# Performance work log

Hardware: AMD Instinct MI355X
Metric: run time of the kernel (lower is better)

## Reference

```python
import jax, jax.numpy as jnp
import numpy as np

B, S, H, NH = 4, 2048, 1024, 16
D = H // NH

def setup_inputs() -> dict:
    key = jax.random.key(0)
    ks = jax.random.split(key, 9)
    sc = 1.0 / np.sqrt(H)
    return {
        "x": jax.random.normal(ks[0], (B, S, H), jnp.float32),
        "Wq": jax.random.normal(ks[1], (H, H), jnp.float32) * sc,
        "bq": jax.random.normal(ks[2], (H,), jnp.float32) * 0.01,
        "Wk": jax.random.normal(ks[3], (H, H), jnp.float32) * sc,
        "bk": jax.random.normal(ks[4], (H,), jnp.float32) * 0.01,
        "Wv": jax.random.normal(ks[5], (H, H), jnp.float32) * sc,
        "bv": jax.random.normal(ks[6], (H,), jnp.float32) * 0.01,
        "Wo": jax.random.normal(ks[7], (H, H), jnp.float32) * sc,
        "bo": jax.random.normal(ks[8], (H,), jnp.float32) * 0.01,
    }

def reference(x, Wq, bq, Wk, bk, Wv, bv, Wo, bo):
    # torch Linear: y = x @ W.T + b
    def proj(x, W, b):
        # [B,S,H] -> [B,NH,S,D]
        y = jnp.einsum('bsh,oh->bso', x, W) + b
        return y.reshape(B, S, NH, D).transpose(0, 2, 1, 3)
    q = proj(x, Wq, bq)
    k = proj(x, Wk, bk)
    v = proj(x, Wv, bv)
    scores = jnp.einsum('bhqd,bhkd->bhqk', q, k) / jnp.sqrt(jnp.float32(D))
    p = jax.nn.softmax(scores, axis=-1)  # [B,NH,S,S]
    o = jnp.einsum('bhqk,bhkd->bhqd', p, v)  # dropout p=0 (eval)
    o = o.transpose(0, 2, 1, 3).reshape(B, S, H)
    return jnp.einsum('bsh,oh->bso', o, Wo) + bo
```

## Files before the change

kernel.cpp:

```cpp
#include <hip/hip_runtime.h>


#define DEV __device__ __forceinline__

typedef __bf16 bf16x8 __attribute__((ext_vector_type(8)));
typedef __bf16 bf16x4 __attribute__((ext_vector_type(4)));
typedef float floatx4 __attribute__((ext_vector_type(4)));

constexpr int Bdim = 4, SS = 2048, HH = 1024, NHH = 16, DD = 64;
constexpr int MM = Bdim * SS;

DEV void async16(const void* g, void* l) {
  __builtin_amdgcn_global_load_lds(
      (const __attribute__((address_space(1))) unsigned int*)g,
      (__attribute__((address_space(3))) unsigned int*)l, 16, 0, 0);
}

DEV int swz2(int r) { return (r ^ (r >> 2)) & 3; }
DEV int swz3(int r) { return (r ^ (r >> 3)) & 7; }

__global__ __launch_bounds__(256) void cast_bf16_kernel(
    const float* __restrict__ x, const float* __restrict__ wq,
    const float* __restrict__ wk, const float* __restrict__ wv,
    const float* __restrict__ wo,
    __bf16* __restrict__ xb, __bf16* __restrict__ wqb, __bf16* __restrict__ wkb,
    __bf16* __restrict__ wvb, __bf16* __restrict__ wob) {
  const float* src; __bf16* dst; int n4;
  switch (blockIdx.z) {
    case 0: src = x;  dst = xb;  n4 = MM * HH / 4; break;
    case 1: src = wq; dst = wqb; n4 = HH * HH / 4; break;
    case 2: src = wk; dst = wkb; n4 = HH * HH / 4; break;
    case 3: src = wv; dst = wvb; n4 = HH * HH / 4; break;
    default: src = wo; dst = wob; n4 = HH * HH / 4; break;
  }
  int stride = gridDim.x * blockDim.x;
  for (int i = blockIdx.x * blockDim.x + threadIdx.x; i < n4; i += stride) {
    float4 v = ((const float4*)src)[i];
    bf16x4 o;
    o[0] = (__bf16)v.x; o[1] = (__bf16)v.y; o[2] = (__bf16)v.z; o[3] = (__bf16)v.w;
    ((bf16x4*)dst)[i] = o;
  }
}

DEV void gemm128(const __bf16* __restrict__ Ablk, const __bf16* __restrict__ Bblk,
                 __bf16* As, __bf16* Bs, floatx4 acc[4][4]) {
  const int t = threadIdx.x;
  const int lane = t & 63, quad = lane >> 4, l16 = lane & 15;
  const int wid = t >> 6;
  const int wm = (wid >> 1) * 64, wn = (wid & 1) * 64;

  const int srow = t >> 2;
  const int sc = t & 3;
  const __bf16* Ag0 = Ablk + (size_t)srow * HH + (sc ^ swz2(srow)) * 8;
  const __bf16* Ag1 = Ablk + (size_t)(srow + 64) * HH + (sc ^ swz2(srow + 64)) * 8;
  const __bf16* Bg0 = Bblk + (size_t)srow * HH + (sc ^ swz2(srow)) * 8;
  const __bf16* Bg1 = Bblk + (size_t)(srow + 64) * HH + (sc ^ swz2(srow + 64)) * 8;
  __bf16* AsW = As + t * 8;
  __bf16* BsW = Bs + t * 8;

  int aoff[4], boff[4];
#pragma unroll
  for (int i = 0; i < 4; ++i) {
    int ra = wm + i * 16 + l16;
    aoff[i] = ra * 32 + (quad ^ swz2(ra)) * 8;
    int rb = wn + i * 16 + l16;
    boff[i] = rb * 32 + (quad ^ swz2(rb)) * 8;
  }

  for (int k0 = 0; k0 < HH; k0 += 32) {
    async16(Ag0 + k0, AsW);
    async16(Ag1 + k0, AsW + 2048);
    async16(Bg0 + k0, BsW);
    async16(Bg1 + k0, BsW + 2048);
    __syncthreads();
    bf16x8 af[4], bfr[4];
#pragma unroll
    for (int i = 0; i < 4; ++i) {
      af[i]  = *(const bf16x8*)&As[aoff[i]];
      bfr[i] = *(const bf16x8*)&Bs[boff[i]];
    }
#pragma unroll
    for (int mi = 0; mi < 4; ++mi)
#pragma unroll
      for (int ni = 0; ni < 4; ++ni)
        acc[mi][ni] = __builtin_amdgcn_mfma_f32_16x16x32_bf16(af[mi], bfr[ni],
                                                              acc[mi][ni], 0, 0, 0);
    __syncthreads();
  }
}

__global__ __launch_bounds__(256) void proj_qkv_kernel(
    const __bf16* __restrict__ xb,
    const __bf16* __restrict__ wqb, const __bf16* __restrict__ wkb,
    const __bf16* __restrict__ wvb,
    const float* __restrict__ bq, const float* __restrict__ bk,
    const float* __restrict__ bv,
    __bf16* __restrict__ Q, __bf16* __restrict__ Kc, __bf16* __restrict__ Vt) {
  __shared__ __align__(16) __bf16 As[128 * 32];
  __shared__ __align__(16) __bf16 Bs[128 * 32];
  const int mode = blockIdx.z;
  const __bf16* W = mode == 0 ? wqb : mode == 1 ? wkb : wvb;
  const float* bias = mode == 0 ? bq : mode == 1 ? bk : bv;
  const int m0 = blockIdx.y * 128, n0 = blockIdx.x * 128;

  floatx4 acc[4][4] = {};
  gemm128(xb + (size_t)m0 * HH, W + (size_t)n0 * HH, As, Bs, acc);

  const int t = threadIdx.x, lane = t & 63, quad = lane >> 4, l16 = lane & 15;
  const int wid = t >> 6, wm = (wid >> 1) * 64, wn = (wid & 1) * 64;
  const float qscale = 0.125f * 1.44269504088896f;
#pragma unroll
  for (int ni = 0; ni < 4; ++ni) {
    int n = n0 + wn + ni * 16 + l16;
    float bval = bias[n];
    int h = n >> 6, d = n & 63;
#pragma unroll
    for (int mi = 0; mi < 4; ++mi) {
#pragma unroll
      for (int r = 0; r < 4; ++r) {
        int m = m0 + wm + mi * 16 + quad * 4 + r;
        int bb = m >> 11, s = m & (SS - 1);
        float v = acc[mi][ni][r] + bval;
        size_t bh = (size_t)(bb * NHH + h);
        if (mode == 0)      Q [(bh * SS + s) * DD + d] = (__bf16)(v * qscale);
        else if (mode == 1) Kc[(bh * SS + s) * DD + d] = (__bf16)v;
        else                Vt[(bh * DD + d) * SS + s] = (__bf16)v;
      }
    }
  }
}

__global__ __launch_bounds__(256) void proj_out_kernel(
    const __bf16* __restrict__ Ob, const __bf16* __restrict__ wob,
    const float* __restrict__ bo, float* __restrict__ out) {
  __shared__ __align__(16) __bf16 As[128 * 32];
  __shared__ __align__(16) __bf16 Bs[128 * 32];
  const int m0 = blockIdx.y * 128, n0 = blockIdx.x * 128;
  floatx4 acc[4][4] = {};
  gemm128(Ob + (size_t)m0 * HH, wob + (size_t)n0 * HH, As, Bs, acc);
  const int t = threadIdx.x, lane = t & 63, quad = lane >> 4, l16 = lane & 15;
  const int wid = t >> 6, wm = (wid >> 1) * 64, wn = (wid & 1) * 64;
#pragma unroll
  for (int ni = 0; ni < 4; ++ni) {
    int n = n0 + wn + ni * 16 + l16;
    float bval = bo[n];
#pragma unroll
    for (int mi = 0; mi < 4; ++mi)
#pragma unroll
      for (int r = 0; r < 4; ++r) {
        int m = m0 + wm + mi * 16 + quad * 4 + r;
        out[(size_t)m * HH + n] = acc[mi][ni][r] + bval;
      }
  }
}

__global__ __launch_bounds__(256, 3) void attn_kernel(
    const __bf16* __restrict__ Q, const __bf16* __restrict__ Kc,
    const __bf16* __restrict__ Vt, __bf16* __restrict__ Ob) {
  __shared__ __align__(16) __bf16 Ks[2][64 * 64];
  __shared__ __align__(16) __bf16 Vs[2][64 * 64];
  __shared__ __align__(16) __bf16 Ps[4 * 32 * 72];

  const int t = threadIdx.x, lane = t & 63, quad = lane >> 4, l16 = lane & 15;
  const int wid = t >> 6;
  const int qt = blockIdx.x, h = blockIdx.y, b = blockIdx.z;
  const size_t bh = (size_t)b * NHH + h;
  const __bf16* Qg = Q + (bh * SS + (size_t)qt * 128) * DD;
  const __bf16* Kg = Kc + bh * SS * DD;
  const __bf16* Vg = Vt + bh * DD * SS;

  const int srow = t >> 3;
  const int sc = t & 7;

  const __bf16* KgA = Kg + (size_t)srow * DD + (sc ^ swz3(srow)) * 8;
  const __bf16* KgB = Kg + (size_t)(srow + 32) * DD + (sc ^ swz3(srow + 32)) * 8;
  const __bf16* VgA = Vg + (size_t)srow * SS + (sc ^ swz3(srow)) * 8;
  const __bf16* VgB = Vg + (size_t)(srow + 32) * SS + (sc ^ swz3(srow + 32)) * 8;

  bf16x8 qf[2][2];
#pragma unroll
  for (int ni = 0; ni < 2; ++ni)
#pragma unroll
    for (int ks = 0; ks < 2; ++ks)
      qf[ni][ks] = *(const bf16x8*)(Qg + (size_t)(wid * 32 + ni * 16 + l16) * DD
                                    + (ks * 4 + quad) * 8);

  floatx4 oacc[2][4] = {};
  float rsum[2] = {0.f, 0.f};

  __bf16* Pw = Ps + wid * (32 * 72);

  int koff[4][2];
#pragma unroll
  for (int mi = 0; mi < 4; ++mi) {
    int r = mi * 16 + l16;
#pragma unroll
    for (int ks = 0; ks < 2; ++ks)
      koff[mi][ks] = r * 64 + ((ks * 4 + quad) ^ swz3(r)) * 8;
  }

  async16(KgA, &Ks[0][t * 8]);
  async16(KgB, &Ks[0][2048 + t * 8]);
  async16(VgA, &Vs[0][t * 8]);
  async16(VgB, &Vs[0][2048 + t * 8]);

  for (int kt = 0; kt < SS / 64; ++kt) {
    const int cur = kt & 1;
    __syncthreads();

    if (kt + 1 < SS / 64) {
      const int kk = (kt + 1) * 64;
      const int nxt = cur ^ 1;
      async16(KgA + (size_t)kk * DD, &Ks[nxt][t * 8]);
      async16(KgB + (size_t)kk * DD, &Ks[nxt][2048 + t * 8]);
      async16(VgA + kk, &Vs[nxt][t * 8]);
      async16(VgB + kk, &Vs[nxt][2048 + t * 8]);
    }

    floatx4 sacc[4][2] = {};
#pragma unroll
    for (int ks = 0; ks < 2; ++ks) {
      bf16x8 kf[4];
#pragma unroll
      for (int mi = 0; mi < 4; ++mi) kf[mi] = *(const bf16x8*)&Ks[cur][koff[mi][ks]];
#pragma unroll
      for (int mi = 0; mi < 4; ++mi)
#pragma unroll
        for (int ni = 0; ni < 2; ++ni)
          sacc[mi][ni] = __builtin_amdgcn_mfma_f32_16x16x32_bf16(kf[mi], qf[ni][ks],
                                                                 sacc[mi][ni], 0, 0, 0);
    }

#pragma unroll
    for (int mi = 0; mi < 4; ++mi)
#pragma unroll
      for (int ni = 0; ni < 2; ++ni) {
        bf16x4 pk;
#pragma unroll
        for (int r = 0; r < 4; ++r) {
          float p = __builtin_amdgcn_exp2f(sacc[mi][ni][r]);
          rsum[ni] += p;
          pk[r] = (__bf16)p;
        }
        *(bf16x4*)&Pw[(ni * 16 + l16) * 72 + mi * 16 + quad * 4] = pk;
      }

#pragma unroll
    for (int ks = 0; ks < 2; ++ks) {
      bf16x8 ap[2], bv8[4];
#pragma unroll
      for (int mi = 0; mi < 2; ++mi)
        ap[mi] = *(const bf16x8*)&Pw[(mi * 16 + l16) * 72 + ks * 32 + quad * 8];
#pragma unroll
      for (int nj = 0; nj < 4; ++nj) bv8[nj] = *(const bf16x8*)&Vs[cur][koff[nj][ks]];
#pragma unroll
      for (int mi = 0; mi < 2; ++mi)
#pragma unroll
        for (int nj = 0; nj < 4; ++nj)
          oacc[mi][nj] = __builtin_amdgcn_mfma_f32_16x16x32_bf16(ap[mi], bv8[nj],
                                                                 oacc[mi][nj], 0, 0, 0);
    }
  }

#pragma unroll
  for (int ni = 0; ni < 2; ++ni) {
    rsum[ni] += __shfl_xor(rsum[ni], 16, 64);
    rsum[ni] += __shfl_xor(rsum[ni], 32, 64);
  }

  const int s0 = qt * 128 + wid * 32;
#pragma unroll
  for (int mi = 0; mi < 2; ++mi) {
#pragma unroll
    for (int r = 0; r < 4; ++r) {
      float inv = 1.f / __shfl(rsum[mi], quad * 4 + r, 64);
      int s = s0 + mi * 16 + quad * 4 + r;
#pragma unroll
      for (int nj = 0; nj < 4; ++nj) {
        int d = nj * 16 + l16;
        Ob[((size_t)b * SS + s) * HH + h * DD + d] = (__bf16)(oacc[mi][nj][r] * inv);
      }
    }
  }
}

extern "C" void kernel_launch(void* const* d_in, const int* in_sizes, int n_in,
                              void* d_out, int out_size, void* d_ws, size_t ws_size,
                              hipStream_t stream) {
  const float* x  = (const float*)d_in[0];
  const float* Wq = (const float*)d_in[1];
  const float* bq = (const float*)d_in[2];
  const float* Wk = (const float*)d_in[3];
  const float* bk = (const float*)d_in[4];
  const float* Wv = (const float*)d_in[5];
  const float* bv = (const float*)d_in[6];
  const float* Wo = (const float*)d_in[7];
  const float* bo = (const float*)d_in[8];
  float* out = (float*)d_out;

  char* ws = (char*)d_ws;
  __bf16* xb  = (__bf16*)(ws);
  __bf16* wqb = (__bf16*)(ws + 16777216);
  __bf16* wkb = (__bf16*)(ws + 18874368);
  __bf16* wvb = (__bf16*)(ws + 20971520);
  __bf16* wob = (__bf16*)(ws + 23068672);
  __bf16* Qb  = (__bf16*)(ws + 25165824);
  __bf16* Kb  = (__bf16*)(ws + 41943040);
  __bf16* Vtb = (__bf16*)(ws + 58720256);
  __bf16* Ob  = (__bf16*)(ws + 75497472);

  cast_bf16_kernel<<<dim3(256, 1, 5), 256, 0, stream>>>(x, Wq, Wk, Wv, Wo,
                                                        xb, wqb, wkb, wvb, wob);
  proj_qkv_kernel<<<dim3(8, 64, 3), 256, 0, stream>>>(xb, wqb, wkb, wvb,
                                                      bq, bk, bv, Qb, Kb, Vtb);
  attn_kernel<<<dim3(16, 16, 4), 256, 0, stream>>>(Qb, Kb, Vtb, Ob);
  proj_out_kernel<<<dim3(8, 64), 256, 0, stream>>>(Ob, wob, bo, out);
}
```

Measured before the change: 323.2 us.

## Double-buffer projection GEMM tiles and fuse QKV into one wide stacked-weight GEMM

Replaces the single-buffered 128x128 GEMM loop with a templated double-buffered version. It prefetches the next K-slice into a second LDS buffer while computing on the current one, which drops one barrier per iteration. The QKV projection now runs as one GEMM over the contiguous stacked Wq/Wk/Wv weights, using 128x256 tiles, and picks the head, mode and bias per output column. This is meant to hide global-load latency and improve A-tile reuse, at the cost of twice the LDS use, more accumulator registers and fewer blocks.

```diff
diff --git a/kernel.cpp b/kernel.cpp
--- a/kernel.cpp
+++ b/kernel.cpp
@@ -42,78 +42,94 @@
   }
 }
 
-DEV void gemm128(const __bf16* __restrict__ Ablk, const __bf16* __restrict__ Bblk,
-                 __bf16* As, __bf16* Bs, floatx4 acc[4][4]) {
+template <int TN>
+DEV void gemm_db(const __bf16* __restrict__ Ablk, const __bf16* __restrict__ Bblk,
+                 __bf16* As, __bf16* Bs, floatx4 acc[4][TN / 32]) {
+  constexpr int NF = TN / 32;
+  constexpr int BGRP = TN / 64;
+  constexpr int BBUF = TN * 32;
   const int t = threadIdx.x;
   const int lane = t & 63, quad = lane >> 4, l16 = lane & 15;
   const int wid = t >> 6;
-  const int wm = (wid >> 1) * 64, wn = (wid & 1) * 64;
-
-  const int srow = t >> 2;
-  const int sc = t & 3;
-  const __bf16* Ag0 = Ablk + (size_t)srow * HH + (sc ^ swz2(srow)) * 8;
-  const __bf16* Ag1 = Ablk + (size_t)(srow + 64) * HH + (sc ^ swz2(srow + 64)) * 8;
-  const __bf16* Bg0 = Bblk + (size_t)srow * HH + (sc ^ swz2(srow)) * 8;
-  const __bf16* Bg1 = Bblk + (size_t)(srow + 64) * HH + (sc ^ swz2(srow + 64)) * 8;
-  __bf16* AsW = As + t * 8;
-  __bf16* BsW = Bs + t * 8;
-
-  int aoff[4], boff[4];
+  const int wm = (wid >> 1) * 64, wn = (wid & 1) * (TN / 2);
+
+  const int srow = t >> 2, sc = t & 3;
+  const __bf16* Ag[2];
+  const __bf16* Bg[BGRP];
+#pragma unroll
+  for (int g = 0; g < 2; ++g)
+    Ag[g] = Ablk + (size_t)(srow + 64 * g) * HH + (sc ^ swz2(srow + 64 * g)) * 8;
+#pragma unroll
+  for (int g = 0; g < BGRP; ++g)
+    Bg[g] = Bblk + (size_t)(srow + 64 * g) * HH + (sc ^ swz2(srow + 64 * g)) * 8;
+
+  int aoff[4], boff[NF];
 #pragma unroll
   for (int i = 0; i < 4; ++i) {
     int ra = wm + i * 16 + l16;
     aoff[i] = ra * 32 + (quad ^ swz2(ra)) * 8;
+  }
+#pragma unroll
+  for (int i = 0; i < NF; ++i) {
     int rb = wn + i * 16 + l16;
     boff[i] = rb * 32 + (quad ^ swz2(rb)) * 8;
   }
 
-  for (int k0 = 0; k0 < HH; k0 += 32) {
-    async16(Ag0 + k0, AsW);
-    async16(Ag1 + k0, AsW + 2048);
-    async16(Bg0 + k0, BsW);
-    async16(Bg1 + k0, BsW + 2048);
+#pragma unroll
+  for (int g = 0; g < 2; ++g) async16(Ag[g], As + g * 2048 + t * 8);
+#pragma unroll
+  for (int g = 0; g < BGRP; ++g) async16(Bg[g], Bs + g * 2048 + t * 8);
+
+  for (int it = 0; it < HH / 32; ++it) {
+    const int cur = it & 1;
     __syncthreads();
-    bf16x8 af[4], bfr[4];
-#pragma unroll
-    for (int i = 0; i < 4; ++i) {
-      af[i]  = *(const bf16x8*)&As[aoff[i]];
-      bfr[i] = *(const bf16x8*)&Bs[boff[i]];
-    }
+
+    if (it + 1 < HH / 32) {
+      const int k = (it + 1) * 32;
+      const int nxt = cur ^ 1;
+#pragma unroll
+      for (int g = 0; g < 2; ++g)
+        async16(Ag[g] + k, As + nxt * 4096 + g * 2048 + t * 8);
+#pragma unroll
+      for (int g = 0; g < BGRP; ++g)
+        async16(Bg[g] + k, Bs + nxt * BBUF + g * 2048 + t * 8);
+    }
+
+    bf16x8 af[4], bfr[NF];
+#pragma unroll
+    for (int i = 0; i < 4; ++i) af[i] = *(const bf16x8*)&As[cur * 4096 + aoff[i]];
+#pragma unroll
+    for (int i = 0; i < NF; ++i) bfr[i] = *(const bf16x8*)&Bs[cur * BBUF + boff[i]];
 #pragma unroll
     for (int mi = 0; mi < 4; ++mi)
 #pragma unroll
-      for (int ni = 0; ni < 4; ++ni)
+      for (int ni = 0; ni < NF; ++ni)
         acc[mi][ni] = __builtin_amdgcn_mfma_f32_16x16x32_bf16(af[mi], bfr[ni],
                                                               acc[mi][ni], 0, 0, 0);
-    __syncthreads();
   }
 }
 
 __global__ __launch_bounds__(256) void proj_qkv_kernel(
-    const __bf16* __restrict__ xb,
-    const __bf16* __restrict__ wqb, const __bf16* __restrict__ wkb,
-    const __bf16* __restrict__ wvb,
+    const __bf16* __restrict__ xb, const __bf16* __restrict__ wstk,
     const float* __restrict__ bq, const float* __restrict__ bk,
     const float* __restrict__ bv,
     __bf16* __restrict__ Q, __bf16* __restrict__ Kc, __bf16* __restrict__ Vt) {
-  __shared__ __align__(16) __bf16 As[128 * 32];
-  __shared__ __align__(16) __bf16 Bs[128 * 32];
-  const int mode = blockIdx.z;
-  const __bf16* W = mode == 0 ? wqb : mode == 1 ? wkb : wvb;
-  const float* bias = mode == 0 ? bq : mode == 1 ? bk : bv;
-  const int m0 = blockIdx.y * 128, n0 = blockIdx.x * 128;
-
-  floatx4 acc[4][4] = {};
-  gemm128(xb + (size_t)m0 * HH, W + (size_t)n0 * HH, As, Bs, acc);
+  __shared__ __align__(16) __bf16 As[2 * 128 * 32];
+  __shared__ __align__(16) __bf16 Bs[2 * 256 * 32];
+  const int m0 = blockIdx.y * 128, n0 = blockIdx.x * 256;
+
+  floatx4 acc[4][8] = {};
+  gemm_db<256>(xb + (size_t)m0 * HH, wstk + (size_t)n0 * HH, As, Bs, acc);
 
   const int t = threadIdx.x, lane = t & 63, quad = lane >> 4, l16 = lane & 15;
-  const int wid = t >> 6, wm = (wid >> 1) * 64, wn = (wid & 1) * 64;
+  const int wid = t >> 6, wm = (wid >> 1) * 64, wn = (wid & 1) * 128;
   const float qscale = 0.125f * 1.44269504088896f;
 #pragma unroll
-  for (int ni = 0; ni < 4; ++ni) {
+  for (int ni = 0; ni < 8; ++ni) {
     int n = n0 + wn + ni * 16 + l16;
-    float bval = bias[n];
-    int h = n >> 6, d = n & 63;
+    int mode = n >> 10, nn = n & 1023;
+    int h = nn >> 6, d = nn & 63;
+    float bval = (mode == 0 ? bq : mode == 1 ? bk : bv)[nn];
 #pragma unroll
     for (int mi = 0; mi < 4; ++mi) {
 #pragma unroll
@@ -133,11 +149,11 @@
 __global__ __launch_bounds__(256) void proj_out_kernel(
     const __bf16* __restrict__ Ob, const __bf16* __restrict__ wob,
     const float* __restrict__ bo, float* __restrict__ out) {
-  __shared__ __align__(16) __bf16 As[128 * 32];
-  __shared__ __align__(16) __bf16 Bs[128 * 32];
+  __shared__ __align__(16) __bf16 As[2 * 128 * 32];
+  __shared__ __align__(16) __bf16 Bs[2 * 128 * 32];
   const int m0 = blockIdx.y * 128, n0 = blockIdx.x * 128;
   floatx4 acc[4][4] = {};
-  gemm128(Ob + (size_t)m0 * HH, wob + (size_t)n0 * HH, As, Bs, acc);
+  gemm_db<128>(Ob + (size_t)m0 * HH, wob + (size_t)n0 * HH, As, Bs, acc);
   const int t = threadIdx.x, lane = t & 63, quad = lane >> 4, l16 = lane & 15;
   const int wid = t >> 6, wm = (wid >> 1) * 64, wn = (wid & 1) * 64;
 #pragma unroll
@@ -311,8 +327,8 @@
 
   cast_bf16_kernel<<<dim3(256, 1, 5), 256, 0, stream>>>(x, Wq, Wk, Wv, Wo,
                                                         xb, wqb, wkb, wvb, wob);
-  proj_qkv_kernel<<<dim3(8, 64, 3), 256, 0, stream>>>(xb, wqb, wkb, wvb,
-                                                      bq, bk, bv, Qb, Kb, Vtb);
+  proj_qkv_kernel<<<dim3(12, 64), 256, 0, stream>>>(xb, wqb, bq, bk, bv,
+                                                    Qb, Kb, Vtb);
   attn_kernel<<<dim3(16, 16, 4), 256, 0, stream>>>(Qb, Kb, Vtb, Ob);
   proj_out_kernel<<<dim3(8, 64), 256, 0, stream>>>(Ob, wob, bo, out);
 }
```

Measured after the change: 355.4 us. +9.9%, slower.

## Double-buffer QKV GEMM, vectorize V stores, and enlarge attention query tile

Applied to the files above, without the earlier changes.

Adds a double-buffered LDS variant of the 128x128 GEMM for the QKV projection, issuing the next K-slice's async loads before computing on the current one, which removes one barrier per iteration. The transposed V epilogue now writes four contiguous bf16 values per store instead of scattered scalars. The attention kernel now gives each wave 64 query rows instead of 32, so each block covers 256 rows and K/V tiles loaded into LDS are reused across twice as many queries. This halves the grid. The cost is more registers, with occupancy lowered from 3 to 2 blocks, and P is processed in two 32-column halves through a smaller staging buffer.

```diff
diff --git a/kernel.cpp b/kernel.cpp
--- a/kernel.cpp
+++ b/kernel.cpp
@@ -42,6 +42,61 @@
   }
 }
 
+DEV void gemm_db128(const __bf16* __restrict__ Ablk, const __bf16* __restrict__ Bblk,
+                    __bf16* As, __bf16* Bs, floatx4 acc[4][4]) {
+  const int t = threadIdx.x;
+  const int lane = t & 63, quad = lane >> 4, l16 = lane & 15;
+  const int wid = t >> 6;
+  const int wm = (wid >> 1) * 64, wn = (wid & 1) * 64;
+
+  const int srow = t >> 2, sc = t & 3;
+  const __bf16* Ag0 = Ablk + (size_t)srow * HH + (sc ^ swz2(srow)) * 8;
+  const __bf16* Ag1 = Ablk + (size_t)(srow + 64) * HH + (sc ^ swz2(srow + 64)) * 8;
+  const __bf16* Bg0 = Bblk + (size_t)srow * HH + (sc ^ swz2(srow)) * 8;
+  const __bf16* Bg1 = Bblk + (size_t)(srow + 64) * HH + (sc ^ swz2(srow + 64)) * 8;
+
+  int aoff[4], boff[4];
+#pragma unroll
+  for (int i = 0; i < 4; ++i) {
+    int ra = wm + i * 16 + l16;
+    aoff[i] = ra * 32 + (quad ^ swz2(ra)) * 8;
+    int rb = wn + i * 16 + l16;
+    boff[i] = rb * 32 + (quad ^ swz2(rb)) * 8;
+  }
+
+  async16(Ag0, As + t * 8);
+  async16(Ag1, As + 2048 + t * 8);
+  async16(Bg0, Bs + t * 8);
+  async16(Bg1, Bs + 2048 + t * 8);
+
+  for (int it = 0; it < HH / 32; ++it) {
+    const int cur = it & 1;
+    __syncthreads();
+
+    if (it + 1 < HH / 32) {
+      const int k = (it + 1) * 32;
+      const int nxt = (cur ^ 1) * 4096;
+      async16(Ag0 + k, As + nxt + t * 8);
+      async16(Ag1 + k, As + nxt + 2048 + t * 8);
+      async16(Bg0 + k, Bs + nxt + t * 8);
+      async16(Bg1 + k, Bs + nxt + 2048 + t * 8);
+    }
+
+    bf16x8 af[4], bfr[4];
+#pragma unroll
+    for (int i = 0; i < 4; ++i) {
+      af[i]  = *(const bf16x8*)&As[cur * 4096 + aoff[i]];
+      bfr[i] = *(const bf16x8*)&Bs[cur * 4096 + boff[i]];
+    }
+#pragma unroll
+    for (int mi = 0; mi < 4; ++mi)
+#pragma unroll
+      for (int ni = 0; ni < 4; ++ni)
+        acc[mi][ni] = __builtin_amdgcn_mfma_f32_16x16x32_bf16(af[mi], bfr[ni],
+                                                              acc[mi][ni], 0, 0, 0);
+  }
+}
+
 DEV void gemm128(const __bf16* __restrict__ Ablk, const __bf16* __restrict__ Bblk,
                  __bf16* As, __bf16* Bs, floatx4 acc[4][4]) {
   const int t = threadIdx.x;
@@ -49,8 +104,7 @@
   const int wid = t >> 6;
   const int wm = (wid >> 1) * 64, wn = (wid & 1) * 64;
 
-  const int srow = t >> 2;
-  const int sc = t & 3;
+  const int srow = t >> 2, sc = t & 3;
   const __bf16* Ag0 = Ablk + (size_t)srow * HH + (sc ^ swz2(srow)) * 8;
   const __bf16* Ag1 = Ablk + (size_t)(srow + 64) * HH + (sc ^ swz2(srow + 64)) * 8;
   const __bf16* Bg0 = Bblk + (size_t)srow * HH + (sc ^ swz2(srow)) * 8;
@@ -96,15 +150,15 @@
     const float* __restrict__ bq, const float* __restrict__ bk,
     const float* __restrict__ bv,
     __bf16* __restrict__ Q, __bf16* __restrict__ Kc, __bf16* __restrict__ Vt) {
-  __shared__ __align__(16) __bf16 As[128 * 32];
-  __shared__ __align__(16) __bf16 Bs[128 * 32];
+  __shared__ __align__(16) __bf16 As[2 * 128 * 32];
+  __shared__ __align__(16) __bf16 Bs[2 * 128 * 32];
   const int mode = blockIdx.z;
   const __bf16* W = mode == 0 ? wqb : mode == 1 ? wkb : wvb;
   const float* bias = mode == 0 ? bq : mode == 1 ? bk : bv;
   const int m0 = blockIdx.y * 128, n0 = blockIdx.x * 128;
 
   floatx4 acc[4][4] = {};
-  gemm128(xb + (size_t)m0 * HH, W + (size_t)n0 * HH, As, Bs, acc);
+  gemm_db128(xb + (size_t)m0 * HH, W + (size_t)n0 * HH, As, Bs, acc);
 
   const int t = threadIdx.x, lane = t & 63, quad = lane >> 4, l16 = lane & 15;
   const int wid = t >> 6, wm = (wid >> 1) * 64, wn = (wid & 1) * 64;
@@ -116,15 +170,21 @@
     int h = n >> 6, d = n & 63;
 #pragma unroll
     for (int mi = 0; mi < 4; ++mi) {
-#pragma unroll
-      for (int r = 0; r < 4; ++r) {
-        int m = m0 + wm + mi * 16 + quad * 4 + r;
-        int bb = m >> 11, s = m & (SS - 1);
-        float v = acc[mi][ni][r] + bval;
-        size_t bh = (size_t)(bb * NHH + h);
-        if (mode == 0)      Q [(bh * SS + s) * DD + d] = (__bf16)(v * qscale);
-        else if (mode == 1) Kc[(bh * SS + s) * DD + d] = (__bf16)v;
-        else                Vt[(bh * DD + d) * SS + s] = (__bf16)v;
+      int mbase = m0 + wm + mi * 16 + quad * 4;
+      int bb = mbase >> 11, sbase = mbase & (SS - 1);
+      size_t bh = (size_t)(bb * NHH + h);
+      if (mode == 2) {
+        bf16x4 pv;
+#pragma unroll
+        for (int r = 0; r < 4; ++r) pv[r] = (__bf16)(acc[mi][ni][r] + bval);
+        *(bf16x4*)&Vt[(bh * DD + d) * SS + sbase] = pv;
+      } else {
+#pragma unroll
+        for (int r = 0; r < 4; ++r) {
+          float v = acc[mi][ni][r] + bval;
+          if (mode == 0) Q [(bh * SS + sbase + r) * DD + d] = (__bf16)(v * qscale);
+          else           Kc[(bh * SS + sbase + r) * DD + d] = (__bf16)v;
+        }
       }
     }
   }
@@ -154,18 +214,18 @@
   }
 }
 
-__global__ __launch_bounds__(256, 3) void attn_kernel(
+__global__ __launch_bounds__(256, 2) void attn_kernel(
     const __bf16* __restrict__ Q, const __bf16* __restrict__ Kc,
     const __bf16* __restrict__ Vt, __bf16* __restrict__ Ob) {
   __shared__ __align__(16) __bf16 Ks[2][64 * 64];
   __shared__ __align__(16) __bf16 Vs[2][64 * 64];
-  __shared__ __align__(16) __bf16 Ps[4 * 32 * 72];
+  __shared__ __align__(16) __bf16 Ps[4 * 64 * 40];
 
   const int t = threadIdx.x, lane = t & 63, quad = lane >> 4, l16 = lane & 15;
   const int wid = t >> 6;
   const int qt = blockIdx.x, h = blockIdx.y, b = blockIdx.z;
   const size_t bh = (size_t)b * NHH + h;
-  const __bf16* Qg = Q + (bh * SS + (size_t)qt * 128) * DD;
+  const __bf16* Qg = Q + (bh * SS + (size_t)qt * 256) * DD;
   const __bf16* Kg = Kc + bh * SS * DD;
   const __bf16* Vg = Vt + bh * DD * SS;
 
@@ -177,18 +237,18 @@
   const __bf16* VgA = Vg + (size_t)srow * SS + (sc ^ swz3(srow)) * 8;
   const __bf16* VgB = Vg + (size_t)(srow + 32) * SS + (sc ^ swz3(srow + 32)) * 8;
 
-  bf16x8 qf[2][2];
-#pragma unroll
-  for (int ni = 0; ni < 2; ++ni)
+  bf16x8 qf[4][2];
+#pragma unroll
+  for (int ni = 0; ni < 4; ++ni)
 #pragma unroll
     for (int ks = 0; ks < 2; ++ks)
-      qf[ni][ks] = *(const bf16x8*)(Qg + (size_t)(wid * 32 + ni * 16 + l16) * DD
+      qf[ni][ks] = *(const bf16x8*)(Qg + (size_t)(wid * 64 + ni * 16 + l16) * DD
                                     + (ks * 4 + quad) * 8);
 
-  floatx4 oacc[2][4] = {};
-  float rsum[2] = {0.f, 0.f};
-
-  __bf16* Pw = Ps + wid * (32 * 72);
+  floatx4 oacc[4][4] = {};
+  float rsum[4] = {0.f, 0.f, 0.f, 0.f};
+
+  __bf16* Pw = Ps + wid * (64 * 40);
 
   int koff[4][2];
 #pragma unroll
@@ -217,7 +277,11 @@
       async16(VgB + kk, &Vs[nxt][2048 + t * 8]);
     }
 
-    floatx4 sacc[4][2] = {};
+    floatx4 sacc[4][4];
+#pragma unroll
+    for (int mi = 0; mi < 4; ++mi)
+#pragma unroll
+      for (int ni = 0; ni < 4; ++ni) sacc[mi][ni] = floatx4{0.f, 0.f, 0.f, 0.f};
 #pragma unroll
     for (int ks = 0; ks < 2; ++ks) {
       bf16x8 kf[4];
@@ -226,59 +290,60 @@
 #pragma unroll
       for (int mi = 0; mi < 4; ++mi)
 #pragma unroll
-        for (int ni = 0; ni < 2; ++ni)
+        for (int ni = 0; ni < 4; ++ni)
           sacc[mi][ni] = __builtin_amdgcn_mfma_f32_16x16x32_bf16(kf[mi], qf[ni][ks],
                                                                  sacc[mi][ni], 0, 0, 0);
     }
 
 #pragma unroll
-    for (int mi = 0; mi < 4; ++mi)
-#pragma unroll
-      for (int ni = 0; ni < 2; ++ni) {
-        bf16x4 pk;
-#pragma unroll
-        for (int r = 0; r < 4; ++r) {
-          float p = __builtin_amdgcn_exp2f(sacc[mi][ni][r]);
-          rsum[ni] += p;
-          pk[r] = (__bf16)p;
+    for (int hf = 0; hf < 2; ++hf) {
+#pragma unroll
+      for (int mh = 0; mh < 2; ++mh) {
+        const int mi = hf * 2 + mh;
+#pragma unroll
+        for (int ni = 0; ni < 4; ++ni) {
+          bf16x4 pk;
+#pragma unroll
+          for (int r = 0; r < 4; ++r) {
+            float p = __builtin_amdgcn_exp2f(sacc[mi][ni][r]);
+            rsum[ni] += p;
+            pk[r] = (__bf16)p;
+          }
+          *(bf16x4*)&Pw[(ni * 16 + l16) * 40 + mh * 16 + quad * 4] = pk;
         }
-        *(bf16x4*)&Pw[(ni * 16 + l16) * 72 + mi * 16 + quad * 4] = pk;
       }
-
-#pragma unroll
-    for (int ks = 0; ks < 2; ++ks) {
-      bf16x8 ap[2], bv8[4];
-#pragma unroll
-      for (int mi = 0; mi < 2; ++mi)
-        ap[mi] = *(const bf16x8*)&Pw[(mi * 16 + l16) * 72 + ks * 32 + quad * 8];
-#pragma unroll
-      for (int nj = 0; nj < 4; ++nj) bv8[nj] = *(const bf16x8*)&Vs[cur][koff[nj][ks]];
-#pragma unroll
-      for (int mi = 0; mi < 2; ++mi)
+      bf16x8 ap[4], bv8[4];
+#pragma unroll
+      for (int mq = 0; mq < 4; ++mq)
+        ap[mq] = *(const bf16x8*)&Pw[(mq * 16 + l16) * 40 + quad * 8];
+#pragma unroll
+      for (int nj = 0; nj < 4; ++nj) bv8[nj] = *(const bf16x8*)&Vs[cur][koff[nj][hf]];
+#pragma unroll
+      for (int mq = 0; mq < 4; ++mq)
 #pragma unroll
         for (int nj = 0; nj < 4; ++nj)
-          oacc[mi][nj] = __builtin_amdgcn_mfma_f32_16x16x32_bf16(ap[mi], bv8[nj],
-                                                                 oacc[mi][nj], 0, 0, 0);
-    }
-  }
-
-#pragma unroll
-  for (int ni = 0; ni < 2; ++ni) {
+          oacc[mq][nj] = __builtin_amdgcn_mfma_f32_16x16x32_bf16(ap[mq], bv8[nj],
+                                                                 oacc[mq][nj], 0, 0, 0);
+    }
+  }
+
+#pragma unroll
+  for (int ni = 0; ni < 4; ++ni) {
     rsum[ni] += __shfl_xor(rsum[ni], 16, 64);
     rsum[ni] += __shfl_xor(rsum[ni], 32, 64);
   }
 
-  const int s0 = qt * 128 + wid * 32;
-#pragma unroll
-  for (int mi = 0; mi < 2; ++mi) {
+  const int s0 = qt * 256 + wid * 64;
+#pragma unroll
+  for (int mq = 0; mq < 4; ++mq) {
 #pragma unroll
     for (int r = 0; r < 4; ++r) {
-      float inv = 1.f / __shfl(rsum[mi], quad * 4 + r, 64);
-      int s = s0 + mi * 16 + quad * 4 + r;
+      float inv = 1.f / __shfl(rsum[mq], quad * 4 + r, 64);
+      int s = s0 + mq * 16 + quad * 4 + r;
 #pragma unroll
       for (int nj = 0; nj < 4; ++nj) {
         int d = nj * 16 + l16;
-        Ob[((size_t)b * SS + s) * HH + h * DD + d] = (__bf16)(oacc[mi][nj][r] * inv);
+        Ob[((size_t)b * SS + s) * HH + h * DD + d] = (__bf16)(oacc[mq][nj][r] * inv);
       }
     }
   }
@@ -313,6 +378,6 @@
                                                         xb, wqb, wkb, wvb, wob);
   proj_qkv_kernel<<<dim3(8, 64, 3), 256, 0, stream>>>(xb, wqb, wkb, wvb,
                                                       bq, bk, bv, Qb, Kb, Vtb);
-  attn_kernel<<<dim3(16, 16, 4), 256, 0, stream>>>(Qb, Kb, Vtb, Ob);
+  attn_kernel<<<dim3(8, 16, 4), 256, 0, stream>>>(Qb, Kb, Vtb, Ob);
   proj_out_kernel<<<dim3(8, 64), 256, 0, stream>>>(Ob, wob, bo, out);
 }
```

Result: faster. 297.1 us (-8.1%).
